# Kernel optimization log

Measured on AMD Instinct MI355X. Metric: run time of the kernel, lower is better.

## Reference

```python
import jax, jax.numpy as jnp
import numpy as np

D_MODEL = 1024
N_HEAD = 16
N_KV = 8
HEAD_DIM = D_MODEL // N_HEAD  # 64
ROPE_BASE = 10000.0


def _rope_tables(T, head_dim):
    inv_freq = 1.0 / (ROPE_BASE ** (jnp.arange(0, head_dim, 2, dtype=jnp.float32) / head_dim))
    pos = jnp.arange(T, dtype=jnp.float32)
    freqs = pos[:, None] * inv_freq[None, :]  # [T, head_dim//2]
    return jnp.sin(freqs), jnp.cos(freqs)


def _apply_rope(x, sin, cos):
    # x: [B, H, T, D]; sin/cos: [T, D//2] broadcast over B,H
    x1 = x[..., ::2]
    x2 = x[..., 1::2]
    y1 = x1 * cos - x2 * sin
    y2 = x1 * sin + x2 * cos
    return jnp.stack([y1, y2], axis=-1).reshape(x.shape)


def setup_inputs() -> dict:
    key = jax.random.key(0)
    ks = jax.random.split(key, 5)
    B, T = 2, 2048
    x = jax.random.normal(ks[0], (B, T, D_MODEL), dtype=jnp.float32)
    std = 0.02
    Wq = std * jax.random.normal(ks[1], (D_MODEL, D_MODEL), dtype=jnp.float32)
    Wk = std * jax.random.normal(ks[2], (N_KV * HEAD_DIM, D_MODEL), dtype=jnp.float32)
    Wv = std * jax.random.normal(ks[3], (N_KV * HEAD_DIM, D_MODEL), dtype=jnp.float32)
    Wo = std * jax.random.normal(ks[4], (D_MODEL, D_MODEL), dtype=jnp.float32)
    return {"x": x, "Wq": Wq, "Wk": Wk, "Wv": Wv, "Wo": Wo}


def reference(x, Wq, Wk, Wv, Wo):
    B, T, _ = x.shape
    G = N_HEAD // N_KV  # query heads per kv head (repeat_interleave grouping)

    # projections (bias-free Linear: x @ W.T)
    q = (x @ Wq.T).reshape(B, T, N_HEAD, HEAD_DIM).transpose(0, 2, 1, 3)  # [B,H,T,D]
    k = (x @ Wk.T).reshape(B, T, N_KV, HEAD_DIM).transpose(0, 2, 1, 3)   # [B,Hkv,T,D]
    v = (x @ Wv.T).reshape(B, T, N_KV, HEAD_DIM).transpose(0, 2, 1, 3)

    sin, cos = _rope_tables(T, HEAD_DIM)
    q = _apply_rope(q, sin, cos)
    k = _apply_rope(k, sin, cos)

    # GQA without materializing repeated K/V: group q heads by kv head.
    # repeat_interleave(dim=1) maps q head h -> kv head h // G.
    qg = q.reshape(B, N_KV, G, T, HEAD_DIM)
    scale = 1.0 / np.sqrt(HEAD_DIM)
    scores = jnp.einsum('bkgtd,bksd->bkgts', qg, k) * scale  # [B,Hkv,G,T,T]
    causal = jnp.tril(jnp.ones((T, T), dtype=bool))
    scores = jnp.where(causal, scores, jnp.float32(-1e30))
    attn = jax.nn.softmax(scores, axis=-1)
    y = jnp.einsum('bkgts,bksd->bkgtd', attn, v)              # [B,Hkv,G,T,D]
    y = y.reshape(B, N_HEAD, T, HEAD_DIM).transpose(0, 2, 1, 3).reshape(B, T, D_MODEL)
    return y @ Wo.T
```

## Files before the change

### kernel.cpp

```cpp
#include <hip/hip_runtime.h>
#include <cstdint>
#include <cstddef>

typedef __attribute__((ext_vector_type(8))) __bf16 bf16x8;
typedef __attribute__((ext_vector_type(4))) __bf16 bf16x4;
typedef __attribute__((ext_vector_type(4))) float f32x4;

#define DEVI __device__ __forceinline__

DEVI void gload_lds16(const void* g, void* l) {
    __builtin_amdgcn_global_load_lds((const __attribute__((address_space(1))) void*)g,
                                     (__attribute__((address_space(3))) void*)l, 16, 0, 0);
}

__global__ __launch_bounds__(256) void cvt_all(
    const float* __restrict__ x, const float* __restrict__ wq,
    const float* __restrict__ wk, const float* __restrict__ wv,
    const float* __restrict__ wo,
    bf16x4* __restrict__ xb, bf16x4* __restrict__ wqb, bf16x4* __restrict__ wkb,
    bf16x4* __restrict__ wvb, bf16x4* __restrict__ wob)
{
    int i = blockIdx.x * 256 + threadIdx.x;
    const int stride = gridDim.x * 256;
    for (; i < 1835008; i += stride) {
        const float4* s; bf16x4* d; int j;
        if (i < 1048576)      { s = (const float4*)x;  d = xb;  j = i; }
        else if (i < 1310720) { s = (const float4*)wq; d = wqb; j = i - 1048576; }
        else if (i < 1441792) { s = (const float4*)wk; d = wkb; j = i - 1310720; }
        else if (i < 1572864) { s = (const float4*)wv; d = wvb; j = i - 1441792; }
        else                  { s = (const float4*)wo; d = wob; j = i - 1572864; }
        float4 v = s[j];
        bf16x4 o = { (__bf16)v.x, (__bf16)v.y, (__bf16)v.z, (__bf16)v.w };
        d[j] = o;
    }
}

__global__ __launch_bounds__(256) void rope_tables(float* __restrict__ sint, float* __restrict__ cost)
{
    int i = blockIdx.x * 256 + threadIdx.x;
    int t = i >> 5, p = i & 31;
    float inv = powf(10000.0f, -(float)p / 32.0f);
    float f = (float)t * inv;
    float s, c;
    sincosf(f, &s, &c);
    sint[i] = s;
    cost[i] = c;
}

__global__ __launch_bounds__(256) void qkv_gemm(
    const __bf16* __restrict__ xb, const __bf16* __restrict__ wqb,
    const __bf16* __restrict__ wkb, const __bf16* __restrict__ wvb,
    const float* __restrict__ sint, const float* __restrict__ cost,
    __bf16* __restrict__ Qo, __bf16* __restrict__ Ko, __bf16* __restrict__ VTo)
{
    __shared__ __bf16 As[2][4096];
    __shared__ __bf16 Bs[2][4096];
    const int tid = threadIdx.x;
    const int lane = tid & 63;
    const int wid = tid >> 6;
    const int wm = (wid >> 1) * 32, wn = (wid & 1) * 32;
    const int m0 = blockIdx.y * 64;
    const int n0 = blockIdx.x * 64;

    const __bf16* bsrc;
    if (n0 < 1024)      bsrc = wqb + (size_t)n0 * 1024;
    else if (n0 < 1536) bsrc = wkb + (size_t)(n0 - 1024) * 1024;
    else                bsrc = wvb + (size_t)(n0 - 1536) * 1024;
    const __bf16* asrc = xb + (size_t)m0 * 1024;

    f32x4 acc[2][2] = {};
    const int sr = tid >> 3, sc = tid & 7;
    const int gsc = (sc ^ (sr & 7)) * 8;

#define STAGE(BUF, K0) do {                                                             \
    gload_lds16(asrc + (size_t)sr * 1024 + (K0) + gsc,        (char*)As[BUF] + sr * 128 + sc * 16); \
    gload_lds16(asrc + (size_t)(sr + 32) * 1024 + (K0) + gsc, (char*)As[BUF] + (sr + 32) * 128 + sc * 16); \
    gload_lds16(bsrc + (size_t)sr * 1024 + (K0) + gsc,        (char*)Bs[BUF] + sr * 128 + sc * 16); \
    gload_lds16(bsrc + (size_t)(sr + 32) * 1024 + (K0) + gsc, (char*)Bs[BUF] + (sr + 32) * 128 + sc * 16); \
} while (0)

    STAGE(0, 0);
    __syncthreads();

#pragma unroll 1
    for (int step = 0; step < 16; ++step) {
        const int cur = step & 1;
        if (step < 15) STAGE(cur ^ 1, (step + 1) * 64);
#pragma unroll
        for (int ks = 0; ks < 2; ++ks) {
            bf16x8 af[2], bfv[2];
#pragma unroll
            for (int i = 0; i < 2; ++i) {
                int ra = wm + i * 16 + (lane & 15);
                af[i] = *(const bf16x8*)((const char*)As[cur] + ra * 128 + (((ks * 4 + (lane >> 4)) ^ (ra & 7)) * 16));
                int rb = wn + i * 16 + (lane & 15);
                bfv[i] = *(const bf16x8*)((const char*)Bs[cur] + rb * 128 + (((ks * 4 + (lane >> 4)) ^ (rb & 7)) * 16));
            }
#pragma unroll
            for (int mi = 0; mi < 2; ++mi)
#pragma unroll
                for (int ni = 0; ni < 2; ++ni)
                    acc[mi][ni] = __builtin_amdgcn_mfma_f32_16x16x32_bf16(af[mi], bfv[ni], acc[mi][ni], 0, 0, 0);
        }
        __syncthreads();
    }
#undef STAGE

    const int rg = lane >> 4, cf = lane & 15;
#pragma unroll
    for (int mi = 0; mi < 2; ++mi) {
#pragma unroll
        for (int ni = 0; ni < 2; ++ni) {
            if (n0 >= 1536) {
                int n = n0 + wn + ni * 16 + cf;
                int nn = n - 1536;
                int kvh = nn >> 6, d = nn & 63;
                int m = m0 + wm + mi * 16 + rg * 4;
                int b = m >> 11;
                int t = m & 2047;
                bf16x4 o;
#pragma unroll
                for (int r = 0; r < 4; ++r) o[r] = (__bf16)acc[mi][ni][r];
                *(bf16x4*)(VTo + ((size_t)(b * 8 + kvh) * 64 + d) * 2048 + t) = o;
            } else {
#pragma unroll
                for (int r = 0; r < 4; ++r) {
                    float v = acc[mi][ni][r];
                    float pv = __shfl_xor(v, 1, 64);
                    int m = m0 + wm + mi * 16 + rg * 4 + r;
                    int n = n0 + wn + ni * 16 + cf;
                    int b = m >> 11;
                    int t = m & 2047;
                    if (n < 1024) {
                        int h = n >> 6, d = n & 63;
                        float s = sint[t * 32 + (d >> 1)], c = cost[t * 32 + (d >> 1)];
                        float o = (d & 1) ? (pv * s + v * c) : (v * c - pv * s);
                        Qo[((size_t)(b * 16 + h) * 2048 + t) * 64 + d] = (__bf16)(o * 0.125f);
                    } else {
                        int nn = n - 1024;
                        int h = nn >> 6, d = nn & 63;
                        float s = sint[t * 32 + (d >> 1)], c = cost[t * 32 + (d >> 1)];
                        float o = (d & 1) ? (pv * s + v * c) : (v * c - pv * s);
                        Ko[((size_t)(b * 8 + h) * 2048 + t) * 64 + d] = (__bf16)o;
                    }
                }
            }
        }
    }
}

__global__ __launch_bounds__(256, 2) void attn_fwd(
    const __bf16* __restrict__ Qg, const __bf16* __restrict__ Kg,
    const __bf16* __restrict__ VTg, __bf16* __restrict__ Yg)
{
    __shared__ char Ks[2][8192];
    __shared__ char Vs[2][8192];
    __shared__ char Pl[8192];
    const int tid = threadIdx.x;
    const int lane = tid & 63;
    const int w = tid >> 6;
    const int lin = blockIdx.x;
    const int xcd = lin & 7, g = (lin >> 3) & 3, i = lin >> 5;
    const int J = (i & 1) ? (i >> 1) : (31 - (i >> 1));
    const int bh = xcd + 8 * g;
    const int b = bh >> 4, h = bh & 15, kvh = h >> 1;
    const size_t qbase = (size_t)(b * 16 + h) * 2048 * 64;
    const size_t kbase = (size_t)(b * 8 + kvh) * 2048 * 64;
    const int rg = lane >> 4, cf = lane & 15;
    char* pw = Pl + w * 2048;

    const int sr = tid >> 3;
    const int sc = tid & 7;
    const int gsc = (sc ^ (sr & 7)) * 8;

    bf16x8 pk0, pk1, pv0, pv1;

    bf16x8 ones;
#pragma unroll
    for (int e = 0; e < 8; ++e) ones[e] = (__bf16)1.0f;

#define PRE(NT) do {                                                                    \
    const int _n0 = (NT) * 64;                                                          \
    pk0 = *(const bf16x8*)(Kg + kbase + (size_t)(_n0 + sr) * 64 + gsc);                 \
    pk1 = *(const bf16x8*)(Kg + kbase + (size_t)(_n0 + sr + 32) * 64 + gsc);            \
    pv0 = *(const bf16x8*)(VTg + kbase + (size_t)sr * 2048 + _n0 + gsc);                \
    pv1 = *(const bf16x8*)(VTg + kbase + (size_t)(sr + 32) * 2048 + _n0 + gsc);         \
} while (0)
#define WRITE_LDS(BUF) do {                                                             \
    *(bf16x8*)(Ks[BUF] + tid * 16) = pk0;                                               \
    *(bf16x8*)(Ks[BUF] + (tid + 256) * 16) = pk1;                                       \
    *(bf16x8*)(Vs[BUF] + tid * 16) = pv0;                                               \
    *(bf16x8*)(Vs[BUF] + (tid + 256) * 16) = pv1;                                       \
} while (0)

    PRE(0);
    WRITE_LDS(0);
    __syncthreads();

    const int r0 = J * 64 + w * 16;
    bf16x8 qf[2];
#pragma unroll
    for (int ks = 0; ks < 2; ++ks)
        qf[ks] = *(const bf16x8*)(Qg + qbase + (size_t)(r0 + cf) * 64 + ks * 32 + rg * 8);
    f32x4 oacc[4] = {}, lacc = {};
    int cur = 0;

#pragma unroll 1
    for (int nt = 0; nt <= J; ++nt) {
        if (nt < J) PRE(nt + 1);

        {
            bf16x8 kf[2][4];
#pragma unroll
            for (int ks = 0; ks < 2; ++ks)
#pragma unroll
                for (int ni = 0; ni < 4; ++ni)
                    kf[ks][ni] = *(const bf16x8*)(Ks[cur] + (ni * 16 + cf) * 128 + (((ks * 4 + rg) ^ (cf & 7)) * 16));

            f32x4 sacc[4] = {};
            __builtin_amdgcn_s_setprio(1);
#pragma unroll
            for (int ks = 0; ks < 2; ++ks)
#pragma unroll
                for (int ni = 0; ni < 4; ++ni)
                    sacc[ni] = __builtin_amdgcn_mfma_f32_16x16x32_bf16(qf[ks], kf[ks][ni], sacc[ni], 0, 0, 0);
            __builtin_amdgcn_s_setprio(0);

            bf16x8 vf[2][4];
#pragma unroll
            for (int ks = 0; ks < 2; ++ks)
#pragma unroll
                for (int df = 0; df < 4; ++df)
                    vf[ks][df] = *(const bf16x8*)(Vs[cur] + (df * 16 + cf) * 128 + (((ks * 4 + rg) ^ (cf & 7)) * 16));

            if (nt == J) {
#pragma unroll
                for (int ni = 0; ni < 4; ++ni)
#pragma unroll
                    for (int r = 0; r < 4; ++r)
                        if (ni * 16 + cf > w * 16 + rg * 4 + r)
                            sacc[ni][r] = -3.0e38f;
            }

#pragma unroll
            for (int ni = 0; ni < 4; ++ni)
#pragma unroll
                for (int r = 0; r < 4; ++r)
                    sacc[ni][r] = __expf(sacc[ni][r]);

#pragma unroll
            for (int ni = 0; ni < 4; ++ni)
#pragma unroll
                for (int r = 0; r < 4; ++r) {
                    int pr = rg * 4 + r;
                    int pc = ni * 16 + cf;
                    *(__bf16*)(pw + pr * 128 + (((pc >> 3) ^ (pr & 7)) * 8 + (pc & 7)) * 2) =
                        (__bf16)sacc[ni][r];
                }

            __builtin_amdgcn_s_setprio(1);
#pragma unroll
            for (int ks = 0; ks < 2; ++ks) {
                bf16x8 pf = *(const bf16x8*)(pw + cf * 128 + (((ks * 4 + rg) ^ (cf & 7)) * 16));
#pragma unroll
                for (int df = 0; df < 4; ++df)
                    oacc[df] = __builtin_amdgcn_mfma_f32_16x16x32_bf16(pf, vf[ks][df], oacc[df], 0, 0, 0);
                lacc = __builtin_amdgcn_mfma_f32_16x16x32_bf16(pf, ones, lacc, 0, 0, 0);
            }
            __builtin_amdgcn_s_setprio(0);
        }

        if (nt == J) {
#pragma unroll
            for (int r = 0; r < 4; ++r) {
                float inv = 1.0f / lacc[r];
                int t = r0 + rg * 4 + r;
#pragma unroll
                for (int df = 0; df < 4; ++df)
                    Yg[((size_t)b * 2048 + t) * 1024 + h * 64 + df * 16 + cf] =
                        (__bf16)(oacc[df][r] * inv);
            }
        }

        if (nt < J) WRITE_LDS(cur ^ 1);
        __syncthreads();
        cur ^= 1;
    }
#undef PRE
#undef WRITE_LDS
}

__global__ __launch_bounds__(256) void out_gemm(
    const __bf16* __restrict__ Yb, const __bf16* __restrict__ Wob, float* __restrict__ outp)
{
    __shared__ __bf16 As[2][8192];
    __shared__ __bf16 Bs[2][4096];
    const int tid = threadIdx.x;
    const int lane = tid & 63;
    const int wid = tid >> 6;
    const int wm = wid * 32;
    const int m0 = blockIdx.y * 128;
    const int n0 = blockIdx.x * 64;
    const __bf16* asrc = Yb + (size_t)m0 * 1024;
    const __bf16* bsrc = Wob + (size_t)n0 * 1024;

    f32x4 acc[2][4] = {};
    const int srow = tid >> 3, schunk = tid & 7;
    const int gc = (schunk ^ (srow & 7)) * 8;

#define STAGE(BUF, K0) do {                                                             \
    _Pragma("unroll") for (int it = 0; it < 4; ++it) {                                  \
        int r = srow + it * 32;                                                         \
        gload_lds16(asrc + (size_t)r * 1024 + (K0) + gc, (char*)As[BUF] + r * 128 + schunk * 16); \
    }                                                                                   \
    _Pragma("unroll") for (int it = 0; it < 2; ++it) {                                  \
        int r = srow + it * 32;                                                         \
        gload_lds16(bsrc + (size_t)r * 1024 + (K0) + gc, (char*)Bs[BUF] + r * 128 + schunk * 16); \
    }                                                                                   \
} while (0)

    STAGE(0, 0);
    __syncthreads();

#pragma unroll 1
    for (int step = 0; step < 16; ++step) {
        const int cur = step & 1;
        if (step < 15) STAGE(cur ^ 1, (step + 1) * 64);
#pragma unroll
        for (int ks = 0; ks < 2; ++ks) {
            bf16x8 af[2], bfv[4];
#pragma unroll
            for (int i = 0; i < 2; ++i) {
                int ra = wm + i * 16 + (lane & 15);
                af[i] = *(const bf16x8*)((const char*)As[cur] + ra * 128 + (((ks * 4 + (lane >> 4)) ^ (ra & 7)) * 16));
            }
#pragma unroll
            for (int i = 0; i < 4; ++i) {
                int rb = i * 16 + (lane & 15);
                bfv[i] = *(const bf16x8*)((const char*)Bs[cur] + rb * 128 + (((ks * 4 + (lane >> 4)) ^ (rb & 7)) * 16));
            }
#pragma unroll
            for (int mi = 0; mi < 2; ++mi)
#pragma unroll
                for (int ni = 0; ni < 4; ++ni)
                    acc[mi][ni] = __builtin_amdgcn_mfma_f32_16x16x32_bf16(af[mi], bfv[ni], acc[mi][ni], 0, 0, 0);
        }
        __syncthreads();
    }
#undef STAGE

    const int rg = lane >> 4, cf = lane & 15;
#pragma unroll
    for (int mi = 0; mi < 2; ++mi)
#pragma unroll
        for (int ni = 0; ni < 4; ++ni)
#pragma unroll
            for (int r = 0; r < 4; ++r) {
                int m = m0 + wm + mi * 16 + rg * 4 + r;
                int n = n0 + ni * 16 + cf;
                outp[(size_t)m * 1024 + n] = acc[mi][ni][r];
            }
}

extern "C" void kernel_launch(void* const* d_in, const int* in_sizes, int n_in,
                              void* d_out, int out_size, void* d_ws, size_t ws_size,
                              hipStream_t stream)
{
    const float* x  = (const float*)d_in[0];
    const float* wq = (const float*)d_in[1];
    const float* wk = (const float*)d_in[2];
    const float* wv = (const float*)d_in[3];
    const float* wo = (const float*)d_in[4];

    char* ws = (char*)d_ws;
    __bf16* xb  = (__bf16*)(ws + 0);
    __bf16* wqb = (__bf16*)(ws + 8388608);
    __bf16* wkb = (__bf16*)(ws + 10485760);
    __bf16* wvb = (__bf16*)(ws + 11534336);
    __bf16* wob = (__bf16*)(ws + 12582912);
    __bf16* Qb  = (__bf16*)(ws + 14680064);
    __bf16* Kb  = (__bf16*)(ws + 23068672);
    __bf16* VTb = (__bf16*)(ws + 31457280);
    __bf16* Yb  = (__bf16*)(ws + 35651584);
    float* sint = (float*)(ws + 44040192);
    float* cost = (float*)(ws + 44302336);
    if (ws_size < 44564480) return;

    cvt_all<<<2048, 256, 0, stream>>>(x, wq, wk, wv, wo,
                                      (bf16x4*)xb, (bf16x4*)wqb, (bf16x4*)wkb,
                                      (bf16x4*)wvb, (bf16x4*)wob);
    rope_tables<<<256, 256, 0, stream>>>(sint, cost);
    qkv_gemm<<<dim3(32, 64), 256, 0, stream>>>(xb, wqb, wkb, wvb, sint, cost, Qb, Kb, VTb);
    attn_fwd<<<1024, 256, 0, stream>>>(Qb, Kb, VTb, Yb);
    out_gemm<<<dim3(16, 32), 256, 0, stream>>>(Yb, wob, (float*)d_out);
}
```

Measured before the change: 101.9 us.

## Double attention query tile to 128 rows per block for K/V reuse

Each attention block now processes 128 query rows (32 per wave, two 16-row MFMA subtiles) instead of 64, so every K/V tile loaded into LDS feeds twice as many MFMAs. The grid halves to 512 blocks, the causal loop runs over 2J+2 key tiles with masking on the last two, and the P scratch buffer doubles. The intent is to cut global and LDS K/V traffic per unit of work. In exchange, register pressure rises (the occupancy hint of 2 is dropped), there are fewer blocks, and the diagonal tiles waste more masked work.

```diff
diff --git a/kernel.cpp b/kernel.cpp
--- a/kernel.cpp
+++ b/kernel.cpp
@@ -149,30 +149,31 @@
     }
 }
 
-__global__ __launch_bounds__(256, 2) void attn_fwd(
+__global__ __launch_bounds__(256) void attn_fwd(
     const __bf16* __restrict__ Qg, const __bf16* __restrict__ Kg,
     const __bf16* __restrict__ VTg, __bf16* __restrict__ Yg)
 {
     __shared__ char Ks[2][8192];
     __shared__ char Vs[2][8192];
-    __shared__ char Pl[8192];
+    __shared__ char Pl[16384];
     const int tid = threadIdx.x;
     const int lane = tid & 63;
     const int w = tid >> 6;
     const int lin = blockIdx.x;
     const int xcd = lin & 7, g = (lin >> 3) & 3, i = lin >> 5;
-    const int J = (i & 1) ? (i >> 1) : (31 - (i >> 1));
+    const int J = (i & 1) ? (i >> 1) : (15 - (i >> 1));
     const int bh = xcd + 8 * g;
     const int b = bh >> 4, h = bh & 15, kvh = h >> 1;
     const size_t qbase = (size_t)(b * 16 + h) * 2048 * 64;
     const size_t kbase = (size_t)(b * 8 + kvh) * 2048 * 64;
     const int rg = lane >> 4, cf = lane & 15;
-    char* pw = Pl + w * 2048;
+    char* pw = Pl + w * 4096;
 
     const int sr = tid >> 3;
     const int sc = tid & 7;
     const int gsc = (sc ^ (sr & 7)) * 8;
 
+    const int ntk = 2 * J + 2;
     bf16x8 pk0, pk1, pv0, pv1;
 
     bf16x8 ones;
@@ -197,17 +198,19 @@
     WRITE_LDS(0);
     __syncthreads();
 
-    const int r0 = J * 64 + w * 16;
-    bf16x8 qf[2];
-#pragma unroll
-    for (int ks = 0; ks < 2; ++ks)
-        qf[ks] = *(const bf16x8*)(Qg + qbase + (size_t)(r0 + cf) * 64 + ks * 32 + rg * 8);
-    f32x4 oacc[4] = {}, lacc = {};
+    const int r0 = J * 128 + w * 32;
+    bf16x8 qf[2][2];
+#pragma unroll
+    for (int mi = 0; mi < 2; ++mi)
+#pragma unroll
+        for (int ks = 0; ks < 2; ++ks)
+            qf[mi][ks] = *(const bf16x8*)(Qg + qbase + (size_t)(r0 + mi * 16 + cf) * 64 + ks * 32 + rg * 8);
+    f32x4 oacc[2][4] = {}, lacc[2] = {};
     int cur = 0;
 
 #pragma unroll 1
-    for (int nt = 0; nt <= J; ++nt) {
-        if (nt < J) PRE(nt + 1);
+    for (int nt = 0; nt < ntk; ++nt) {
+        if (nt < ntk - 1) PRE(nt + 1);
 
         {
             bf16x8 kf[2][4];
@@ -217,13 +220,15 @@
                 for (int ni = 0; ni < 4; ++ni)
                     kf[ks][ni] = *(const bf16x8*)(Ks[cur] + (ni * 16 + cf) * 128 + (((ks * 4 + rg) ^ (cf & 7)) * 16));
 
-            f32x4 sacc[4] = {};
+            f32x4 sacc[2][4] = {};
             __builtin_amdgcn_s_setprio(1);
 #pragma unroll
             for (int ks = 0; ks < 2; ++ks)
 #pragma unroll
-                for (int ni = 0; ni < 4; ++ni)
-                    sacc[ni] = __builtin_amdgcn_mfma_f32_16x16x32_bf16(qf[ks], kf[ks][ni], sacc[ni], 0, 0, 0);
+                for (int mi = 0; mi < 2; ++mi)
+#pragma unroll
+                    for (int ni = 0; ni < 4; ++ni)
+                        sacc[mi][ni] = __builtin_amdgcn_mfma_f32_16x16x32_bf16(qf[mi][ks], kf[ks][ni], sacc[mi][ni], 0, 0, 0);
             __builtin_amdgcn_s_setprio(0);
 
             bf16x8 vf[2][4];
@@ -233,56 +238,73 @@
                 for (int df = 0; df < 4; ++df)
                     vf[ks][df] = *(const bf16x8*)(Vs[cur] + (df * 16 + cf) * 128 + (((ks * 4 + rg) ^ (cf & 7)) * 16));
 
-            if (nt == J) {
+            if (nt >= 2 * J) {
+                const int koff = (nt - 2 * J) * 64;
+#pragma unroll
+                for (int mi = 0; mi < 2; ++mi)
+#pragma unroll
+                    for (int ni = 0; ni < 4; ++ni)
+#pragma unroll
+                        for (int r = 0; r < 4; ++r)
+                            if (koff + ni * 16 + cf > w * 32 + mi * 16 + rg * 4 + r)
+                                sacc[mi][ni][r] = -3.0e38f;
+            }
+
+#pragma unroll
+            for (int mi = 0; mi < 2; ++mi)
 #pragma unroll
                 for (int ni = 0; ni < 4; ++ni)
 #pragma unroll
                     for (int r = 0; r < 4; ++r)
-                        if (ni * 16 + cf > w * 16 + rg * 4 + r)
-                            sacc[ni][r] = -3.0e38f;
-            }
-
-#pragma unroll
-            for (int ni = 0; ni < 4; ++ni)
-#pragma unroll
-                for (int r = 0; r < 4; ++r)
-                    sacc[ni][r] = __expf(sacc[ni][r]);
-
-#pragma unroll
-            for (int ni = 0; ni < 4; ++ni)
-#pragma unroll
-                for (int r = 0; r < 4; ++r) {
-                    int pr = rg * 4 + r;
-                    int pc = ni * 16 + cf;
-                    *(__bf16*)(pw + pr * 128 + (((pc >> 3) ^ (pr & 7)) * 8 + (pc & 7)) * 2) =
-                        (__bf16)sacc[ni][r];
+                        sacc[mi][ni][r] = __expf(sacc[mi][ni][r]);
+
+#pragma unroll
+            for (int mi = 0; mi < 2; ++mi)
+#pragma unroll
+                for (int ni = 0; ni < 4; ++ni)
+#pragma unroll
+                    for (int r = 0; r < 4; ++r) {
+                        int pr = mi * 16 + rg * 4 + r;
+                        int pc = ni * 16 + cf;
+                        *(__bf16*)(pw + pr * 128 + (((pc >> 3) ^ (pr & 7)) * 8 + (pc & 7)) * 2) =
+                            (__bf16)sacc[mi][ni][r];
+                    }
+
+            __builtin_amdgcn_s_setprio(1);
+#pragma unroll
+            for (int ks = 0; ks < 2; ++ks) {
+                bf16x8 pf[2];
+#pragma unroll
+                for (int mi = 0; mi < 2; ++mi) {
+                    int pr = mi * 16 + cf;
+                    pf[mi] = *(const bf16x8*)(pw + pr * 128 + (((ks * 4 + rg) ^ (pr & 7)) * 16));
                 }
-
-            __builtin_amdgcn_s_setprio(1);
-#pragma unroll
-            for (int ks = 0; ks < 2; ++ks) {
-                bf16x8 pf = *(const bf16x8*)(pw + cf * 128 + (((ks * 4 + rg) ^ (cf & 7)) * 16));
-#pragma unroll
-                for (int df = 0; df < 4; ++df)
-                    oacc[df] = __builtin_amdgcn_mfma_f32_16x16x32_bf16(pf, vf[ks][df], oacc[df], 0, 0, 0);
-                lacc = __builtin_amdgcn_mfma_f32_16x16x32_bf16(pf, ones, lacc, 0, 0, 0);
+#pragma unroll
+                for (int mi = 0; mi < 2; ++mi) {
+#pragma unroll
+                    for (int df = 0; df < 4; ++df)
+                        oacc[mi][df] = __builtin_amdgcn_mfma_f32_16x16x32_bf16(pf[mi], vf[ks][df], oacc[mi][df], 0, 0, 0);
+                    lacc[mi] = __builtin_amdgcn_mfma_f32_16x16x32_bf16(pf[mi], ones, lacc[mi], 0, 0, 0);
+                }
             }
             __builtin_amdgcn_s_setprio(0);
         }
 
-        if (nt == J) {
-#pragma unroll
-            for (int r = 0; r < 4; ++r) {
-                float inv = 1.0f / lacc[r];
-                int t = r0 + rg * 4 + r;
-#pragma unroll
-                for (int df = 0; df < 4; ++df)
-                    Yg[((size_t)b * 2048 + t) * 1024 + h * 64 + df * 16 + cf] =
-                        (__bf16)(oacc[df][r] * inv);
-            }
+        if (nt == ntk - 1) {
+#pragma unroll
+            for (int mi = 0; mi < 2; ++mi)
+#pragma unroll
+                for (int r = 0; r < 4; ++r) {
+                    float inv = 1.0f / lacc[mi][r];
+                    int t = r0 + mi * 16 + rg * 4 + r;
+#pragma unroll
+                    for (int df = 0; df < 4; ++df)
+                        Yg[((size_t)b * 2048 + t) * 1024 + h * 64 + df * 16 + cf] =
+                            (__bf16)(oacc[mi][df][r] * inv);
+                }
         }
 
-        if (nt < J) WRITE_LDS(cur ^ 1);
+        if (nt < ntk - 1) WRITE_LDS(cur ^ 1);
         __syncthreads();
         cur ^= 1;
     }
@@ -391,6 +413,6 @@
                                       (bf16x4*)wvb, (bf16x4*)wob);
     rope_tables<<<256, 256, 0, stream>>>(sint, cost);
     qkv_gemm<<<dim3(32, 64), 256, 0, stream>>>(xb, wqb, wkb, wvb, sint, cost, Qb, Kb, VTb);
-    attn_fwd<<<1024, 256, 0, stream>>>(Qb, Kb, VTb, Yb);
+    attn_fwd<<<512, 256, 0, stream>>>(Qb, Kb, VTb, Yb);
     out_gemm<<<dim3(16, 32), 256, 0, stream>>>(Yb, wob, (float*)d_out);
 }
```

Measured after the change: 114.6 us. 12.5% more time.
